# Performance work log

Measured on AMD Instinct MI355X. Metric: run time of the kernel, lower is better.

Reference implementation:

```python
import jax, jax.numpy as jnp
import numpy as np

B, N, D = 64, 2048, 256
EPS = 1e-05


def setup_inputs() -> dict:
    key = jax.random.key(0)
    k1, k2 = jax.random.split(key)
    x = jax.random.normal(k1, (B, N, D), dtype=jnp.float32)
    lengths = jax.random.randint(k2, (B,), 1, N + 1, dtype=jnp.int32)
    weights = jnp.ones((D,), dtype=jnp.float32)
    biases = jnp.zeros((D,), dtype=jnp.float32)
    return {"x": x, "lengths": lengths, "weights": weights, "biases": biases}


def reference(x, lengths, weights, biases):
    # mask: [B, N, 1], 1.0 for valid set elements (idx < length)
    mask = (jnp.arange(N)[None, :] < lengths[:, None])[..., None].astype(x.dtype)
    denom = (lengths.astype(x.dtype) * D)  # [B]
    xm = x * mask
    means = jnp.sum(xm, axis=(1, 2)) / denom                      # [B]
    x_centered = (xm - means[:, None, None]) * mask               # [B,N,D]
    variances = jnp.sum(x_centered * x_centered, axis=(1, 2)) / denom  # [B]
    x_norm = x_centered / (jnp.sqrt(variances)[:, None, None] + EPS)
    # F.linear(x, diag_embed(w), b) == x * w + b (elementwise per-feature affine)
    out = (x_norm * weights + biases) * mask
    return out
```

## Files before the change

### kernel.cpp

```cpp
#include <hip/hip_runtime.h>


#define BB 64
#define NN 2048
#define DD 256
#define EPSV 1e-5f
#define CHUNKS 8
#define ROWS_PER_CHUNK (NN / CHUNKS)

__global__ __launch_bounds__(256) void setnorm_partials(
    const float* __restrict__ x, const int* __restrict__ lengths,
    float* __restrict__ partials) {
  const int c = blockIdx.x;
  const int b = blockIdx.y;
  const int len = lengths[b];
  const int rowBase = c * ROWS_PER_CHUNK;
  int validRows = len - rowBase;
  if (validRows > ROWS_PER_CHUNK) validRows = ROWS_PER_CHUNK;

  float sum = 0.f, sumsq = 0.f;
  if (validRows > 0) {
    const float4* p =
        (const float4*)(x + ((size_t)b * NN + (size_t)rowBase) * DD);
    const int n4 = validRows * (DD / 4);
    for (int i = threadIdx.x; i < n4; i += blockDim.x) {
      float4 v = p[i];
      sum += v.x + v.y + v.z + v.w;
      sumsq += v.x * v.x + v.y * v.y + v.z * v.z + v.w * v.w;
    }
  }
  #pragma unroll
  for (int off = 32; off > 0; off >>= 1) {
    sum += __shfl_down(sum, off, 64);
    sumsq += __shfl_down(sumsq, off, 64);
  }
  __shared__ float ssum[4], ssq[4];
  const int wave = threadIdx.x >> 6;
  const int lane = threadIdx.x & 63;
  if (lane == 0) { ssum[wave] = sum; ssq[wave] = sumsq; }
  __syncthreads();
  if (threadIdx.x == 0) {
    float ts = 0.f, tq = 0.f;
    #pragma unroll
    for (int w = 0; w < 4; ++w) { ts += ssum[w]; tq += ssq[w]; }
    partials[(b * CHUNKS + c) * 2 + 0] = ts;
    partials[(b * CHUNKS + c) * 2 + 1] = tq;
  }
}

__global__ __launch_bounds__(64) void setnorm_finalize(
    const float* __restrict__ partials, const int* __restrict__ lengths,
    float* __restrict__ stats) {
  const int b = threadIdx.x;
  if (b < BB) {
    float s = 0.f, q = 0.f;
    #pragma unroll
    for (int c = 0; c < CHUNKS; ++c) {
      s += partials[(b * CHUNKS + c) * 2 + 0];
      q += partials[(b * CHUNKS + c) * 2 + 1];
    }
    const float denom = (float)lengths[b] * (float)DD;
    const float mean = s / denom;
    float var = q / denom - mean * mean;
    var = fmaxf(var, 0.f);
    const float inv = 1.f / (sqrtf(var) + EPSV);
    stats[b * 2 + 0] = mean;
    stats[b * 2 + 1] = inv;
  }
}

__global__ __launch_bounds__(256) void setnorm_normalize(
    const float* __restrict__ x, const int* __restrict__ lengths,
    const float* __restrict__ weights, const float* __restrict__ biases,
    const float* __restrict__ stats, float* __restrict__ out) {
  const int idx4 = blockIdx.x * blockDim.x + threadIdx.x;
  const int b = idx4 >> 17;
  const int rem = idx4 & 131071;
  const int row = rem >> 6;
  const int d4 = rem & 63;
  const int len = lengths[b];
  float4 o;
  if (row < len) {
    const float mean = stats[b * 2 + 0];
    const float inv = stats[b * 2 + 1];
    const float4 v = ((const float4*)x)[idx4];
    const float4 w = ((const float4*)weights)[d4];
    const float4 bi = ((const float4*)biases)[d4];
    o.x = (v.x - mean) * inv * w.x + bi.x;
    o.y = (v.y - mean) * inv * w.y + bi.y;
    o.z = (v.z - mean) * inv * w.z + bi.z;
    o.w = (v.w - mean) * inv * w.w + bi.w;
  } else {
    o.x = 0.f; o.y = 0.f; o.z = 0.f; o.w = 0.f;
  }
  ((float4*)out)[idx4] = o;
}

extern "C" void kernel_launch(void* const* d_in, const int* in_sizes, int n_in,
                              void* d_out, int out_size, void* d_ws, size_t ws_size,
                              hipStream_t stream) {
  const float* x = (const float*)d_in[0];
  const int* lengths = (const int*)d_in[1];
  const float* weights = (const float*)d_in[2];
  const float* biases = (const float*)d_in[3];
  float* out = (float*)d_out;

  float* partials = (float*)d_ws;
  float* stats = partials + BB * CHUNKS * 2;

  dim3 g1(CHUNKS, BB);
  setnorm_partials<<<g1, 256, 0, stream>>>(x, lengths, partials);
  setnorm_finalize<<<1, 64, 0, stream>>>(partials, lengths, stats);
  const int total4 = BB * NN * DD / 4;
  setnorm_normalize<<<total4 / 256, 256, 0, stream>>>(x, lengths, weights,
                                                      biases, stats, out);
}
```

Measured before the change: 251.1 us.

## Fold finalize into normalize kernel, raise reduction chunks, use nontemporal stores

```diff
diff --git a/kernel.cpp b/kernel.cpp
--- a/kernel.cpp
+++ b/kernel.cpp
@@ -5,8 +5,10 @@
 #define NN 2048
 #define DD 256
 #define EPSV 1e-5f
-#define CHUNKS 8
+#define CHUNKS 32
 #define ROWS_PER_CHUNK (NN / CHUNKS)
+
+typedef float f32x4 __attribute__((ext_vector_type(4)));
 
 __global__ __launch_bounds__(256) void setnorm_partials(
     const float* __restrict__ x, const int* __restrict__ lengths,
@@ -20,11 +22,11 @@
 
   float sum = 0.f, sumsq = 0.f;
   if (validRows > 0) {
-    const float4* p =
-        (const float4*)(x + ((size_t)b * NN + (size_t)rowBase) * DD);
+    const f32x4* p =
+        (const f32x4*)(x + ((size_t)b * NN + (size_t)rowBase) * DD);
     const int n4 = validRows * (DD / 4);
-    for (int i = threadIdx.x; i < n4; i += blockDim.x) {
-      float4 v = p[i];
+    for (int i = threadIdx.x; i < n4; i += 256) {
+      f32x4 v = p[i];
       sum += v.x + v.y + v.z + v.w;
       sumsq += v.x * v.x + v.y * v.y + v.z * v.z + v.w * v.w;
     }
@@ -48,52 +50,53 @@
   }
 }
 
-__global__ __launch_bounds__(64) void setnorm_finalize(
-    const float* __restrict__ partials, const int* __restrict__ lengths,
-    float* __restrict__ stats) {
-  const int b = threadIdx.x;
-  if (b < BB) {
-    float s = 0.f, q = 0.f;
-    #pragma unroll
-    for (int c = 0; c < CHUNKS; ++c) {
-      s += partials[(b * CHUNKS + c) * 2 + 0];
-      q += partials[(b * CHUNKS + c) * 2 + 1];
-    }
-    const float denom = (float)lengths[b] * (float)DD;
-    const float mean = s / denom;
-    float var = q / denom - mean * mean;
-    var = fmaxf(var, 0.f);
-    const float inv = 1.f / (sqrtf(var) + EPSV);
-    stats[b * 2 + 0] = mean;
-    stats[b * 2 + 1] = inv;
-  }
-}
-
-__global__ __launch_bounds__(256) void setnorm_normalize(
+__global__ __launch_bounds__(256) void setnorm_norm(
     const float* __restrict__ x, const int* __restrict__ lengths,
     const float* __restrict__ weights, const float* __restrict__ biases,
-    const float* __restrict__ stats, float* __restrict__ out) {
-  const int idx4 = blockIdx.x * blockDim.x + threadIdx.x;
+    const float* __restrict__ partials, float* __restrict__ out) {
+  const int idx4 = blockIdx.x * 256 + threadIdx.x;
   const int b = idx4 >> 17;
   const int rem = idx4 & 131071;
   const int row = rem >> 6;
   const int d4 = rem & 63;
+
+  __shared__ float s_mean, s_inv;
+  if (threadIdx.x < 64) {
+    float s = 0.f, q = 0.f;
+    if (threadIdx.x < CHUNKS) {
+      s = partials[(b * CHUNKS + threadIdx.x) * 2 + 0];
+      q = partials[(b * CHUNKS + threadIdx.x) * 2 + 1];
+    }
+    #pragma unroll
+    for (int off = 16; off > 0; off >>= 1) {
+      s += __shfl_down(s, off, 64);
+      q += __shfl_down(q, off, 64);
+    }
+    if (threadIdx.x == 0) {
+      const float denom = (float)lengths[b] * (float)DD;
+      const float mean = s / denom;
+      float var = q / denom - mean * mean;
+      var = fmaxf(var, 0.f);
+      s_mean = mean;
+      s_inv = 1.f / (sqrtf(var) + EPSV);
+    }
+  }
+  __syncthreads();
+
   const int len = lengths[b];
-  float4 o;
+  f32x4 o = {0.f, 0.f, 0.f, 0.f};
   if (row < len) {
-    const float mean = stats[b * 2 + 0];
-    const float inv = stats[b * 2 + 1];
-    const float4 v = ((const float4*)x)[idx4];
-    const float4 w = ((const float4*)weights)[d4];
-    const float4 bi = ((const float4*)biases)[d4];
+    const float mean = s_mean;
+    const float inv = s_inv;
+    const f32x4 v = ((const f32x4*)x)[idx4];
+    const f32x4 w = ((const f32x4*)weights)[d4];
+    const f32x4 bi = ((const f32x4*)biases)[d4];
     o.x = (v.x - mean) * inv * w.x + bi.x;
     o.y = (v.y - mean) * inv * w.y + bi.y;
     o.z = (v.z - mean) * inv * w.z + bi.z;
     o.w = (v.w - mean) * inv * w.w + bi.w;
-  } else {
-    o.x = 0.f; o.y = 0.f; o.z = 0.f; o.w = 0.f;
   }
-  ((float4*)out)[idx4] = o;
+  __builtin_nontemporal_store(o, ((f32x4*)out) + idx4);
 }
 
 extern "C" void kernel_launch(void* const* d_in, const int* in_sizes, int n_in,
@@ -106,12 +109,10 @@
   float* out = (float*)d_out;
 
   float* partials = (float*)d_ws;
-  float* stats = partials + BB * CHUNKS * 2;
 
   dim3 g1(CHUNKS, BB);
   setnorm_partials<<<g1, 256, 0, stream>>>(x, lengths, partials);
-  setnorm_finalize<<<1, 64, 0, stream>>>(partials, lengths, stats);
   const int total4 = BB * NN * DD / 4;
-  setnorm_normalize<<<total4 / 256, 256, 0, stream>>>(x, lengths, weights,
-                                                      biases, stats, out);
+  setnorm_norm<<<total4 / 256, 256, 0, stream>>>(x, lengths, weights, biases,
+                                                 partials, out);
 }
```

Result: faster. 231.5 us (-7.8%).
